# Kernel tuning notes

Hardware: AMD Instinct MI355X
Metric: run time of the kernel (lower is better)

The kernel has to match this reference:

```python
import jax, jax.numpy as jnp
import numpy as np

DIM = 1024
N_SLOTS = 64
SCALE = 1.0 / np.sqrt(DIM).astype(np.float32)


def _orthogonal(key, n, scale):
    a = jax.random.normal(key, (n, n), dtype=jnp.float32)
    q, r = jnp.linalg.qr(a)
    q = q * jnp.sign(jnp.diag(r))[None, :]
    return q * scale


def setup_inputs() -> dict:
    key = jax.random.key(0)
    ks = jax.random.split(key, 8)
    B, T, D = 16, 1024, DIM
    s = 1.0 / np.sqrt(D)
    x = jax.random.normal(ks[0], (B, T, D), dtype=jnp.float32)
    in_proj_w = jax.random.uniform(ks[1], (D, D), minval=-s, maxval=s, dtype=jnp.float32)
    out_proj_w = jax.random.uniform(ks[2], (D, D), minval=-s, maxval=s, dtype=jnp.float32)
    gate_proj_w = jax.random.uniform(ks[3], (D, D), minval=-s, maxval=s, dtype=jnp.float32)
    W_x = jax.random.uniform(ks[4], (D, D), minval=-s, maxval=s, dtype=jnp.float32)
    W_h = _orthogonal(ks[5], D, 0.9)
    W_write = jax.random.uniform(ks[6], (D, D), minval=-s, maxval=s, dtype=jnp.float32)
    b_h = jnp.zeros((D,), dtype=jnp.float32)
    return {"x": x, "in_proj_w": in_proj_w, "out_proj_w": out_proj_w,
            "gate_proj_w": gate_proj_w, "W_x": W_x, "W_h": W_h,
            "W_write": W_write, "b_h": b_h}


def _cell(x_proj, W_x, W_h, W_write, b_h):
    # x_proj: [B, T, D]
    B, T, D = x_proj.shape
    wx_all = jnp.einsum('btd,ed->bte', x_proj, W_x)  # precomputed W_x @ x
    h_tape0 = jnp.zeros((B, N_SLOTS, D), dtype=x_proj.dtype)
    h_work0 = jnp.zeros((B, D), dtype=x_proj.dtype)

    def step(carry, wx_t):
        h_tape, h_work = carry
        Rh = h_work @ W_h.T
        read_attn = jax.nn.softmax(jnp.einsum('bd,bnd->bn', h_work, h_tape) * SCALE, axis=-1)
        read = jnp.einsum('bn,bnd->bd', read_attn, h_tape)
        h_work = jnp.tanh(Rh + wx_t + read + b_h)
        write_val = h_work @ W_write.T
        write_attn = jax.nn.softmax(jnp.einsum('bd,bnd->bn', h_work, h_tape) * SCALE, axis=-1)
        wa = write_attn[..., None]  # [B, N, 1]
        h_tape = (1.0 - wa) * h_tape + wa * write_val[:, None, :]
        return (h_tape, h_work), h_work

    (h_tape_f, h_work_f), h_work_all = jax.lax.scan(
        step, (h_tape0, h_work0), jnp.swapaxes(wx_all, 0, 1))
    return jnp.swapaxes(h_work_all, 0, 1), h_tape_f, h_work_f


def reference(x, in_proj_w, out_proj_w, gate_proj_w, W_x, W_h, W_write, b_h):
    x_proj = x @ in_proj_w.T  # [B, T, D]
    h_work_all, h_tape_f, h_work_f = _cell(x_proj, W_x, W_h, W_write, b_h)
    gate = jax.nn.silu(x @ gate_proj_w.T)
    output = (h_work_all * gate) @ out_proj_w.T
    return output, h_tape_f, h_work_f
```

## Files before the change

kernel.cpp:

```cpp
#include <hip/hip_runtime.h>
#include <math.h>

#define SCALE_F 0.03125f

template<bool BT, int EPI>
__global__ __launch_bounds__(256) void gemm_nt(const float* __restrict__ A,
                                               const float* __restrict__ Bm,
                                               float* __restrict__ C,
                                               int M, int N, int K) {
  __shared__ float As[32][68];
  __shared__ float Bs[32][68];
  const int tid = threadIdx.x;
  const int n0 = blockIdx.x * 64;
  const int m0 = blockIdx.y * 64;
  const int i0 = (tid >> 4) * 4;
  const int j0 = (tid & 15) * 4;
  float acc[4][4] = {};

  for (int k0 = 0; k0 < K; k0 += 32) {
#pragma unroll
    for (int s = 0; s < 2; ++s) {
      int id = tid + 256 * s;
      int r = id >> 3, c4 = id & 7;
      float4 v = *(const float4*)&A[(size_t)(m0 + r) * K + k0 + c4 * 4];
      As[c4 * 4 + 0][r] = v.x; As[c4 * 4 + 1][r] = v.y;
      As[c4 * 4 + 2][r] = v.z; As[c4 * 4 + 3][r] = v.w;
    }
    if (BT) {
#pragma unroll
      for (int s = 0; s < 2; ++s) {
        int id = tid + 256 * s;
        int r = id >> 3, c4 = id & 7;
        float4 v = *(const float4*)&Bm[(size_t)(n0 + r) * K + k0 + c4 * 4];
        Bs[c4 * 4 + 0][r] = v.x; Bs[c4 * 4 + 1][r] = v.y;
        Bs[c4 * 4 + 2][r] = v.z; Bs[c4 * 4 + 3][r] = v.w;
      }
    } else {
#pragma unroll
      for (int s = 0; s < 2; ++s) {
        int id = tid + 256 * s;
        int kk = id >> 4, c4 = id & 15;
        float4 v = *(const float4*)&Bm[(size_t)(k0 + kk) * N + n0 + c4 * 4];
        *(float4*)&Bs[kk][c4 * 4] = v;
      }
    }
    __syncthreads();
#pragma unroll
    for (int kk = 0; kk < 32; ++kk) {
      float4 a = *(const float4*)&As[kk][i0];
      float4 b = *(const float4*)&Bs[kk][j0];
      float av[4] = {a.x, a.y, a.z, a.w};
      float bv[4] = {b.x, b.y, b.z, b.w};
#pragma unroll
      for (int ii = 0; ii < 4; ++ii)
#pragma unroll
        for (int jj = 0; jj < 4; ++jj)
          acc[ii][jj] = fmaf(av[ii], bv[jj], acc[ii][jj]);
    }
    __syncthreads();
  }

#pragma unroll
  for (int ii = 0; ii < 4; ++ii) {
    float4 v;
    float* vp = (float*)&v;
#pragma unroll
    for (int jj = 0; jj < 4; ++jj) {
      float x = acc[ii][jj];
      if (EPI == 1) x = x / (1.0f + __expf(-x));
      vp[jj] = x;
    }
    *(float4*)&C[(size_t)(m0 + i0 + ii) * N + n0 + j0] = v;
  }
}

__device__ __forceinline__ float ald(const float* p) {
  return __hip_atomic_load(p, __ATOMIC_RELAXED, __HIP_MEMORY_SCOPE_AGENT);
}
__device__ __forceinline__ void ast(float* p, float v) {
  __hip_atomic_store(p, v, __ATOMIC_RELAXED, __HIP_MEMORY_SCOPE_AGENT);
}
__device__ __forceinline__ int ildi(const int* p) {
  return __hip_atomic_load(p, __ATOMIC_RELAXED, __HIP_MEMORY_SCOPE_AGENT);
}
__device__ __forceinline__ void iast(int* p, int v) {
  __hip_atomic_store(p, v, __ATOMIC_RELAXED, __HIP_MEMORY_SCOPE_AGENT);
}

#define TIDX(n, e) ((n) * 64 + (((e) + (n)) & 63))

#define REP16(M) M(0) M(1) M(2) M(3) M(4) M(5) M(6) M(7) M(8) M(9) M(10) \
  M(11) M(12) M(13) M(14) M(15)

#define WDECL(i) float4 w##i;
#define WLOAD(i) w##i = wb4[(i)];
#define MV(i) { float4 hh; \
  hh = *(const float4*)&hs0[4*(i)]; \
  a0=fmaf(w##i.x,hh.x,a0); a0=fmaf(w##i.y,hh.y,a0); a0=fmaf(w##i.z,hh.z,a0); a0=fmaf(w##i.w,hh.w,a0); \
  hh = *(const float4*)&hs1[4*(i)]; \
  a1=fmaf(w##i.x,hh.x,a1); a1=fmaf(w##i.y,hh.y,a1); a1=fmaf(w##i.z,hh.z,a1); a1=fmaf(w##i.w,hh.w,a1); \
  hh = *(const float4*)&hs2[4*(i)]; \
  a2=fmaf(w##i.x,hh.x,a2); a2=fmaf(w##i.y,hh.y,a2); a2=fmaf(w##i.z,hh.z,a2); a2=fmaf(w##i.w,hh.w,a2); \
  hh = *(const float4*)&hs3[4*(i)]; \
  a3=fmaf(w##i.x,hh.x,a3); a3=fmaf(w##i.y,hh.y,a3); a3=fmaf(w##i.z,hh.z,a3); a3=fmaf(w##i.w,hh.w,a3); }

__global__ __launch_bounds__(512) void scan_kernel(
    const float* __restrict__ W_h, const float* __restrict__ W_wr,
    const float* __restrict__ b_h, const float* __restrict__ gate,
    float* __restrict__ wx,
    float* __restrict__ ps_g,
    float* __restrict__ Rh_g,
    float* __restrict__ wv_g,
    float* __restrict__ qp_g,
    float* __restrict__ h_g,
    float* __restrict__ tape_out,
    int* __restrict__ flags) {
  const int tid  = threadIdx.x;
  const int wg   = blockIdx.x;
  const int g    = wg >> 6;
  const int idx  = wg & 63;
  const int b_loc = idx >> 4;
  const int es   = idx & 15;
  const int gb   = g * 4;
  const int bsel = gb + b_loc;
  const int E0   = es * 64;
  const int R0   = es * 64 + b_loc * 16;
  const int wave = tid >> 6;
  const int lane = tid & 63;
  const int rl   = tid >> 4;
  const int cs   = tid & 15;
  const int nwr  = tid >> 3;
  const int ksb  = tid & 7;

  __shared__ float h_sh[4 * 1088];
  __shared__ float tape_l[64 * 64];
  __shared__ float qtmp[4][16];
  __shared__ float ws_lds[64], wa_lds[64], attn_lds[64];
  __shared__ float wv_lds[64], Rh_lds[64], h_own[64], read_lds[64];
  __shared__ float q_lds;
  __shared__ volatile float lds_pad[12288];
  lds_pad[tid] = 0.0f;

  int* fA = flags;
  int* fB = flags + 256;

  const float* Wmat = (rl < 16) ? W_h : W_wr;
  const float4* wb4 =
      (const float4*)(Wmat + (size_t)(R0 + (rl & 15)) * 1024 + cs * 64);
  REP16(WDECL)
  REP16(WLOAD)

  for (int i = tid; i < 4096; i += 512) tape_l[i] = 0.0f;

  float bh_r = 0.0f;
  if (wave == 0) bh_r = b_h[E0 + lane];
  __syncthreads();

  if (wave == 0) {
    size_t xi = (size_t)bsel * 1048576 + E0 + lane;
    float hv = tanhf(wx[xi] + bh_r);
    h_own[lane] = hv;
    ast(&h_g[bsel * 1024 + E0 + lane], hv);
    wx[xi] = hv * gate[xi];
  }
  if (tid < 64) ast(&ps_g[bsel * 1024 + es * 64 + tid], 0.0f);
  __syncthreads();
  if (tid == 0) {
    asm volatile("s_waitcnt vmcnt(0) lgkmcnt(0)" ::: "memory");
    iast(&fA[wg], 1);
  }

  const float* hs0 = &h_sh[0 * 1088 + cs * 68];
  const float* hs1 = &h_sh[1 * 1088 + cs * 68];
  const float* hs2 = &h_sh[2 * 1088 + cs * 68];
  const float* hs3 = &h_sh[3 * 1088 + cs * 68];

  for (int j = 1; j <= 1024; ++j) {
    const bool last = (j == 1024);

    if (wave == 0) {
      const int* f = &fA[g * 64];
      for (;;) {
        int v = ildi(&f[lane]);
        if (__all(v >= j)) break;
        __builtin_amdgcn_s_sleep(2);
      }
    }
    __syncthreads();

#pragma unroll
    for (int r = 0; r < 8; ++r) {
      int i = tid + r * 512;
      int bl = i >> 10, d = i & 1023;
      h_sh[bl * 1088 + (d >> 6) * 68 + (d & 63)] =
          ald(&h_g[(size_t)(gb + bl) * 1024 + d]);
    }
    float p0 = ald(&ps_g[bsel * 1024 + (ksb * 2) * 64 + nwr]);
    float p1 = ald(&ps_g[bsel * 1024 + (ksb * 2 + 1) * 64 + nwr]);
    float wxv = 0.0f, gv = 0.0f;
    size_t xj = 0;
    if (wave == 0 && !last) {
      xj  = (size_t)bsel * 1048576 + (size_t)j * 1024 + E0 + lane;
      wxv = wx[xj];
      gv  = gate[xj];
    }
    __syncthreads();

    float a0 = 0.0f, a1 = 0.0f, a2 = 0.0f, a3 = 0.0f;
    REP16(MV)
#pragma unroll
    for (int m = 1; m < 16; m <<= 1) {
      a0 += __shfl_xor(a0, m); a1 += __shfl_xor(a1, m);
      a2 += __shfl_xor(a2, m); a3 += __shfl_xor(a3, m);
    }
    if (cs == 0) {
      const int grow = R0 + (rl & 15);
      if (rl < 16) {
        ast(&Rh_g[(size_t)(gb + 0) * 1024 + grow], a0);
        ast(&Rh_g[(size_t)(gb + 1) * 1024 + grow], a1);
        ast(&Rh_g[(size_t)(gb + 2) * 1024 + grow], a2);
        ast(&Rh_g[(size_t)(gb + 3) * 1024 + grow], a3);
      } else {
        ast(&wv_g[(size_t)(gb + 0) * 1024 + grow], a0);
        ast(&wv_g[(size_t)(gb + 1) * 1024 + grow], a1);
        ast(&wv_g[(size_t)(gb + 2) * 1024 + grow], a2);
        ast(&wv_g[(size_t)(gb + 3) * 1024 + grow], a3);
        const int hoff = (grow >> 6) * 68 + (grow & 63);
        qtmp[0][rl - 16] = a0 * h_sh[0 * 1088 + hoff];
        qtmp[1][rl - 16] = a1 * h_sh[1 * 1088 + hoff];
        qtmp[2][rl - 16] = a2 * h_sh[2 * 1088 + hoff];
        qtmp[3][rl - 16] = a3 * h_sh[3 * 1088 + hoff];
      }
    }
    {
      float s = p0 + p1;
      s += __shfl_xor(s, 1);
      s += __shfl_xor(s, 2);
      s += __shfl_xor(s, 4);
      if (ksb == 0) ws_lds[nwr] = s;
    }
    __syncthreads();

    if (wave == 0) {
      float s = ws_lds[lane] * SCALE_F;
      float m = s;
#pragma unroll
      for (int off = 1; off < 64; off <<= 1) m = fmaxf(m, __shfl_xor(m, off));
      float ex = __expf(s - m);
      float sum = ex;
#pragma unroll
      for (int off = 1; off < 64; off <<= 1) sum += __shfl_xor(sum, off);
      wa_lds[lane] = ex / sum;
    } else if (wave == 1) {
      int bq = lane >> 4, k = lane & 15;
      float s = qtmp[bq][k];
      s += __shfl_xor(s, 1); s += __shfl_xor(s, 2);
      s += __shfl_xor(s, 4); s += __shfl_xor(s, 8);
      if (k == 0) ast(&qp_g[(size_t)(gb + bq) * 64 + idx], s);
    }
    __syncthreads();
    if (tid == 0) {
      asm volatile("s_waitcnt vmcnt(0) lgkmcnt(0)" ::: "memory");
      iast(&fB[wg], j);
    }

    if (wave == 0) {
      const int* f = &fB[g * 64];
      for (;;) {
        int v = ildi(&f[lane]);
        if (__all(v >= j)) break;
        __builtin_amdgcn_s_sleep(2);
      }
    }
    __syncthreads();

    if (wave == 2) {
      wv_lds[lane] = ald(&wv_g[(size_t)bsel * 1024 + E0 + lane]);
    } else if (wave == 3) {
      Rh_lds[lane] = ald(&Rh_g[(size_t)bsel * 1024 + E0 + lane]);
    } else if (wave == 1) {
      float qv = ald(&qp_g[(size_t)bsel * 64 + lane]);
#pragma unroll
      for (int off = 1; off < 64; off <<= 1) qv += __shfl_xor(qv, off);
      if (lane == 0) q_lds = qv;
    }
    __syncthreads();

    if (wave == 0 && !last) {
      float wsr = ws_lds[lane];
      float rs = fmaf(wa_lds[lane], q_lds - wsr, wsr) * SCALE_F;
      float m = rs;
#pragma unroll
      for (int off = 1; off < 64; off <<= 1) m = fmaxf(m, __shfl_xor(m, off));
      float ex = __expf(rs - m);
      float sum = ex;
#pragma unroll
      for (int off = 1; off < 64; off <<= 1) sum += __shfl_xor(sum, off);
      attn_lds[lane] = ex / sum;
    }
    {
      float wa = wa_lds[nwr];
#pragma unroll
      for (int i = 0; i < 8; ++i) {
        int e = ksb * 8 + i;
        int ix = TIDX(nwr, e);
        float t = tape_l[ix];
        tape_l[ix] = fmaf(wa, wv_lds[e] - t, t);
      }
    }
    if (last) break;
    __syncthreads();

    {
      int ge = tid >> 3, gn = tid & 7;
      float gsum = 0.0f;
#pragma unroll
      for (int i = 0; i < 8; ++i) {
        int n = gn * 8 + i;
        gsum = fmaf(attn_lds[n], tape_l[TIDX(n, ge)], gsum);
      }
      gsum += __shfl_xor(gsum, 1);
      gsum += __shfl_xor(gsum, 2);
      gsum += __shfl_xor(gsum, 4);
      if (gn == 0) read_lds[ge] = gsum;
    }
    __syncthreads();

    if (wave == 0) {
      float hv = tanhf(Rh_lds[lane] + wxv + read_lds[lane] + bh_r);
      h_own[lane] = hv;
      ast(&h_g[bsel * 1024 + E0 + lane], hv);
      wx[xj] = hv * gv;
    }
    __syncthreads();

    {
      float s = 0.0f;
#pragma unroll
      for (int i = 0; i < 8; ++i) {
        int e = ksb * 8 + i;
        s = fmaf(h_own[e], tape_l[TIDX(nwr, e)], s);
      }
      s += __shfl_xor(s, 1);
      s += __shfl_xor(s, 2);
      s += __shfl_xor(s, 4);
      if (ksb == 0) ast(&ps_g[bsel * 1024 + es * 64 + nwr], s);
    }
    __syncthreads();
    if (tid == 0) {
      asm volatile("s_waitcnt vmcnt(0) lgkmcnt(0)" ::: "memory");
      iast(&fA[wg], j + 1);
    }
  }

#pragma unroll
  for (int i = 0; i < 8; ++i) {
    int e = ksb * 8 + i;
    tape_out[(size_t)(bsel * 64 + nwr) * 1024 + E0 + e] = tape_l[TIDX(nwr, e)];
  }
}

extern "C" void kernel_launch(void* const* d_in, const int* in_sizes, int n_in,
                              void* d_out, int out_size, void* d_ws, size_t ws_size,
                              hipStream_t stream) {
  (void)in_sizes; (void)n_in; (void)out_size; (void)ws_size;
  const float* x      = (const float*)d_in[0];
  const float* in_w   = (const float*)d_in[1];
  const float* out_w  = (const float*)d_in[2];
  const float* gate_w = (const float*)d_in[3];
  const float* W_x    = (const float*)d_in[4];
  const float* W_h    = (const float*)d_in[5];
  const float* W_wr   = (const float*)d_in[6];
  const float* b_h    = (const float*)d_in[7];

  float* out  = (float*)d_out;
  float* tape = out + (size_t)16 * 1024 * 1024;
  float* hfin = tape + (size_t)16 * 64 * 1024;

  float* ws = (float*)d_ws;
  float* ps_g = ws;
  float* Rh_g = ws + 16384;
  float* wv_g = ws + 32768;
  float* qp_g = ws + 49152;
  int*   flg  = (int*)(ws + 50176);
  float* M1   = ws;
  float* wx   = ws + (1 << 20);

  float* gate = out;

  dim3 blk(256);
  gemm_nt<false, 0><<<dim3(16, 16), blk, 0, stream>>>(W_x, in_w, M1, 1024, 1024, 1024);
  gemm_nt<true, 1><<<dim3(16, 256), blk, 0, stream>>>(x, gate_w, gate, 16384, 1024, 1024);
  gemm_nt<true, 0><<<dim3(16, 256), blk, 0, stream>>>(x, M1, wx, 16384, 1024, 1024);
  hipMemsetAsync(flg, 0, 2048, stream);
  scan_kernel<<<256, 512, 0, stream>>>(W_h, W_wr, b_h, gate, wx, ps_g, Rh_g,
                                       wv_g, qp_g, hfin, tape, flg);
  gemm_nt<true, 0><<<dim3(16, 256), blk, 0, stream>>>(wx, out_w, out, 16384, 1024, 1024);
}
```

Baseline: 12.99 ms.

## Double scan block to 1024 threads with transposed h layout and per-wave row matvec

The persistent scan kernel now runs 1024 threads per block instead of 512. Each wave owns two weight rows, with lane-strided weights held in registers, and reduces across the full wave. h is stored in LDS transposed and interleaved by batch, stride 6, so each lane reads all four batch values with two float2 loads. The tape update, read and score loops are re-split across the doubled thread count. The goal is to shorten per-step latency on the serial recurrence, at the cost of longer cross-lane reductions, more threads at each barrier, and register pressure under the 1024-thread launch bound.

```diff
diff --git a/kernel.cpp b/kernel.cpp
--- a/kernel.cpp
+++ b/kernel.cpp
@@ -89,22 +89,23 @@
 
 #define TIDX(n, e) ((n) * 64 + (((e) + (n)) & 63))
 
-#define REP16(M) M(0) M(1) M(2) M(3) M(4) M(5) M(6) M(7) M(8) M(9) M(10) \
-  M(11) M(12) M(13) M(14) M(15)
-
-#define WDECL(i) float4 w##i;
-#define WLOAD(i) w##i = wb4[(i)];
-#define MV(i) { float4 hh; \
-  hh = *(const float4*)&hs0[4*(i)]; \
-  a0=fmaf(w##i.x,hh.x,a0); a0=fmaf(w##i.y,hh.y,a0); a0=fmaf(w##i.z,hh.z,a0); a0=fmaf(w##i.w,hh.w,a0); \
-  hh = *(const float4*)&hs1[4*(i)]; \
-  a1=fmaf(w##i.x,hh.x,a1); a1=fmaf(w##i.y,hh.y,a1); a1=fmaf(w##i.z,hh.z,a1); a1=fmaf(w##i.w,hh.w,a1); \
-  hh = *(const float4*)&hs2[4*(i)]; \
-  a2=fmaf(w##i.x,hh.x,a2); a2=fmaf(w##i.y,hh.y,a2); a2=fmaf(w##i.z,hh.z,a2); a2=fmaf(w##i.w,hh.w,a2); \
-  hh = *(const float4*)&hs3[4*(i)]; \
-  a3=fmaf(w##i.x,hh.x,a3); a3=fmaf(w##i.y,hh.y,a3); a3=fmaf(w##i.z,hh.z,a3); a3=fmaf(w##i.w,hh.w,a3); }
-
-__global__ __launch_bounds__(512) void scan_kernel(
+#define WQL(R, Q) \
+  float4 w##R##Q = make_float4(Wp[(R) * 1024 + 64 * (4 * (Q) + 0)], \
+                               Wp[(R) * 1024 + 64 * (4 * (Q) + 1)], \
+                               Wp[(R) * 1024 + 64 * (4 * (Q) + 2)], \
+                               Wp[(R) * 1024 + 64 * (4 * (Q) + 3)]);
+
+#define MVC(Q, IDX, COMP) { \
+  const int cc = l + 64 * (4 * (Q) + (IDX)); \
+  float2 hA = *(const float2*)&h_t[6 * cc]; \
+  float2 hB = *(const float2*)&h_t[6 * cc + 2]; \
+  a00 = fmaf(w0##Q.COMP, hA.x, a00); a01 = fmaf(w0##Q.COMP, hA.y, a01); \
+  a02 = fmaf(w0##Q.COMP, hB.x, a02); a03 = fmaf(w0##Q.COMP, hB.y, a03); \
+  a10 = fmaf(w1##Q.COMP, hA.x, a10); a11 = fmaf(w1##Q.COMP, hA.y, a11); \
+  a12 = fmaf(w1##Q.COMP, hB.x, a12); a13 = fmaf(w1##Q.COMP, hB.y, a13); }
+#define MVQ(Q) MVC(Q, 0, x) MVC(Q, 1, y) MVC(Q, 2, z) MVC(Q, 3, w)
+
+__global__ __launch_bounds__(1024) void scan_kernel(
     const float* __restrict__ W_h, const float* __restrict__ W_wr,
     const float* __restrict__ b_h, const float* __restrict__ gate,
     float* __restrict__ wx,
@@ -125,16 +126,15 @@
   const int bsel = gb + b_loc;
   const int E0   = es * 64;
   const int R0   = es * 64 + b_loc * 16;
-  const int wave = tid >> 6;
+  const int w    = tid >> 6;
   const int lane = tid & 63;
-  const int rl   = tid >> 4;
-  const int cs   = tid & 15;
-  const int nwr  = tid >> 3;
-  const int ksb  = tid & 7;
-
-  __shared__ float h_sh[4 * 1088];
+  const int l    = lane;
+  const int nw2  = tid >> 4;
+  const int ks2  = tid & 15;
+
+  __shared__ float h_t[1024 * 6];
   __shared__ float tape_l[64 * 64];
-  __shared__ float qtmp[4][16];
+  __shared__ float qtmp[8][4];
   __shared__ float ws_lds[64], wa_lds[64], attn_lds[64];
   __shared__ float wv_lds[64], Rh_lds[64], h_own[64], read_lds[64];
   __shared__ float q_lds;
@@ -144,19 +144,18 @@
   int* fA = flags;
   int* fB = flags + 256;
 
-  const float* Wmat = (rl < 16) ? W_h : W_wr;
-  const float4* wb4 =
-      (const float4*)(Wmat + (size_t)(R0 + (rl & 15)) * 1024 + cs * 64);
-  REP16(WDECL)
-  REP16(WLOAD)
-
-  for (int i = tid; i < 4096; i += 512) tape_l[i] = 0.0f;
+  const float* Wp = ((w < 8) ? W_h : W_wr)
+                    + (size_t)(R0 + ((w & 7) << 1)) * 1024 + l;
+  WQL(0, 0) WQL(0, 1) WQL(0, 2) WQL(0, 3)
+  WQL(1, 0) WQL(1, 1) WQL(1, 2) WQL(1, 3)
+
+  for (int i = tid; i < 4096; i += 1024) tape_l[i] = 0.0f;
 
   float bh_r = 0.0f;
-  if (wave == 0) bh_r = b_h[E0 + lane];
+  if (w == 0) bh_r = b_h[E0 + lane];
   __syncthreads();
 
-  if (wave == 0) {
+  if (w == 0) {
     size_t xi = (size_t)bsel * 1048576 + E0 + lane;
     float hv = tanhf(wx[xi] + bh_r);
     h_own[lane] = hv;
@@ -170,15 +169,10 @@
     iast(&fA[wg], 1);
   }
 
-  const float* hs0 = &h_sh[0 * 1088 + cs * 68];
-  const float* hs1 = &h_sh[1 * 1088 + cs * 68];
-  const float* hs2 = &h_sh[2 * 1088 + cs * 68];
-  const float* hs3 = &h_sh[3 * 1088 + cs * 68];
-
   for (int j = 1; j <= 1024; ++j) {
     const bool last = (j == 1024);
 
-    if (wave == 0) {
+    if (w == 0) {
       const int* f = &fA[g * 64];
       for (;;) {
         int v = ildi(&f[lane]);
@@ -189,59 +183,65 @@
     __syncthreads();
 
 #pragma unroll
-    for (int r = 0; r < 8; ++r) {
-      int i = tid + r * 512;
+    for (int r = 0; r < 4; ++r) {
+      int i = tid + r * 1024;
       int bl = i >> 10, d = i & 1023;
-      h_sh[bl * 1088 + (d >> 6) * 68 + (d & 63)] =
-          ald(&h_g[(size_t)(gb + bl) * 1024 + d]);
-    }
-    float p0 = ald(&ps_g[bsel * 1024 + (ksb * 2) * 64 + nwr]);
-    float p1 = ald(&ps_g[bsel * 1024 + (ksb * 2 + 1) * 64 + nwr]);
+      h_t[6 * d + bl] = ald(&h_g[(size_t)(gb + bl) * 1024 + d]);
+    }
+    float p0 = 0.0f, p1 = 0.0f;
+    if (tid < 512) {
+      int nwr = tid >> 3, ksb = tid & 7;
+      p0 = ald(&ps_g[bsel * 1024 + (ksb * 2) * 64 + nwr]);
+      p1 = ald(&ps_g[bsel * 1024 + (ksb * 2 + 1) * 64 + nwr]);
+    }
     float wxv = 0.0f, gv = 0.0f;
     size_t xj = 0;
-    if (wave == 0 && !last) {
+    if (w == 0 && !last) {
       xj  = (size_t)bsel * 1048576 + (size_t)j * 1024 + E0 + lane;
       wxv = wx[xj];
       gv  = gate[xj];
     }
     __syncthreads();
 
-    float a0 = 0.0f, a1 = 0.0f, a2 = 0.0f, a3 = 0.0f;
-    REP16(MV)
-#pragma unroll
-    for (int m = 1; m < 16; m <<= 1) {
-      a0 += __shfl_xor(a0, m); a1 += __shfl_xor(a1, m);
-      a2 += __shfl_xor(a2, m); a3 += __shfl_xor(a3, m);
-    }
-    if (cs == 0) {
-      const int grow = R0 + (rl & 15);
-      if (rl < 16) {
-        ast(&Rh_g[(size_t)(gb + 0) * 1024 + grow], a0);
-        ast(&Rh_g[(size_t)(gb + 1) * 1024 + grow], a1);
-        ast(&Rh_g[(size_t)(gb + 2) * 1024 + grow], a2);
-        ast(&Rh_g[(size_t)(gb + 3) * 1024 + grow], a3);
-      } else {
-        ast(&wv_g[(size_t)(gb + 0) * 1024 + grow], a0);
-        ast(&wv_g[(size_t)(gb + 1) * 1024 + grow], a1);
-        ast(&wv_g[(size_t)(gb + 2) * 1024 + grow], a2);
-        ast(&wv_g[(size_t)(gb + 3) * 1024 + grow], a3);
-        const int hoff = (grow >> 6) * 68 + (grow & 63);
-        qtmp[0][rl - 16] = a0 * h_sh[0 * 1088 + hoff];
-        qtmp[1][rl - 16] = a1 * h_sh[1 * 1088 + hoff];
-        qtmp[2][rl - 16] = a2 * h_sh[2 * 1088 + hoff];
-        qtmp[3][rl - 16] = a3 * h_sh[3 * 1088 + hoff];
-      }
-    }
-    {
+    float a00 = 0.0f, a01 = 0.0f, a02 = 0.0f, a03 = 0.0f;
+    float a10 = 0.0f, a11 = 0.0f, a12 = 0.0f, a13 = 0.0f;
+    MVQ(0) MVQ(1) MVQ(2) MVQ(3)
+    if (tid < 512) {
+      int nwr = tid >> 3, ksb = tid & 7;
       float s = p0 + p1;
       s += __shfl_xor(s, 1);
       s += __shfl_xor(s, 2);
       s += __shfl_xor(s, 4);
       if (ksb == 0) ws_lds[nwr] = s;
     }
-    __syncthreads();
-
-    if (wave == 0) {
+#pragma unroll
+    for (int m = 1; m < 64; m <<= 1) {
+      a00 += __shfl_xor(a00, m); a01 += __shfl_xor(a01, m);
+      a02 += __shfl_xor(a02, m); a03 += __shfl_xor(a03, m);
+      a10 += __shfl_xor(a10, m); a11 += __shfl_xor(a11, m);
+      a12 += __shfl_xor(a12, m); a13 += __shfl_xor(a13, m);
+    }
+    if (l == 0) {
+      const int gr0 = R0 + ((w & 7) << 1);
+      float* dst = (w < 8) ? Rh_g : wv_g;
+      ast(&dst[(size_t)(gb + 0) * 1024 + gr0], a00);
+      ast(&dst[(size_t)(gb + 1) * 1024 + gr0], a01);
+      ast(&dst[(size_t)(gb + 2) * 1024 + gr0], a02);
+      ast(&dst[(size_t)(gb + 3) * 1024 + gr0], a03);
+      ast(&dst[(size_t)(gb + 0) * 1024 + gr0 + 1], a10);
+      ast(&dst[(size_t)(gb + 1) * 1024 + gr0 + 1], a11);
+      ast(&dst[(size_t)(gb + 2) * 1024 + gr0 + 1], a12);
+      ast(&dst[(size_t)(gb + 3) * 1024 + gr0 + 1], a13);
+      if (w >= 8) {
+        qtmp[w - 8][0] = a00 * h_t[6 * gr0 + 0] + a10 * h_t[6 * (gr0 + 1) + 0];
+        qtmp[w - 8][1] = a01 * h_t[6 * gr0 + 1] + a11 * h_t[6 * (gr0 + 1) + 1];
+        qtmp[w - 8][2] = a02 * h_t[6 * gr0 + 2] + a12 * h_t[6 * (gr0 + 1) + 2];
+        qtmp[w - 8][3] = a03 * h_t[6 * gr0 + 3] + a13 * h_t[6 * (gr0 + 1) + 3];
+      }
+    }
+    __syncthreads();
+
+    if (w == 0) {
       float s = ws_lds[lane] * SCALE_F;
       float m = s;
 #pragma unroll
@@ -251,12 +251,15 @@
 #pragma unroll
       for (int off = 1; off < 64; off <<= 1) sum += __shfl_xor(sum, off);
       wa_lds[lane] = ex / sum;
-    } else if (wave == 1) {
-      int bq = lane >> 4, k = lane & 15;
-      float s = qtmp[bq][k];
-      s += __shfl_xor(s, 1); s += __shfl_xor(s, 2);
-      s += __shfl_xor(s, 4); s += __shfl_xor(s, 8);
-      if (k == 0) ast(&qp_g[(size_t)(gb + bq) * 64 + idx], s);
+    } else if (w == 1) {
+      if (lane < 32) {
+        int bq = lane >> 3, ww = lane & 7;
+        float s = qtmp[ww][bq];
+        s += __shfl_xor(s, 1);
+        s += __shfl_xor(s, 2);
+        s += __shfl_xor(s, 4);
+        if (ww == 0) ast(&qp_g[(size_t)(gb + bq) * 64 + idx], s);
+      }
     }
     __syncthreads();
     if (tid == 0) {
@@ -264,7 +267,7 @@
       iast(&fB[wg], j);
     }
 
-    if (wave == 0) {
+    if (w == 0) {
       const int* f = &fB[g * 64];
       for (;;) {
         int v = ildi(&f[lane]);
@@ -274,11 +277,11 @@
     }
     __syncthreads();
 
-    if (wave == 2) {
+    if (w == 2) {
       wv_lds[lane] = ald(&wv_g[(size_t)bsel * 1024 + E0 + lane]);
-    } else if (wave == 3) {
+    } else if (w == 3) {
       Rh_lds[lane] = ald(&Rh_g[(size_t)bsel * 1024 + E0 + lane]);
-    } else if (wave == 1) {
+    } else if (w == 1) {
       float qv = ald(&qp_g[(size_t)bsel * 64 + lane]);
 #pragma unroll
       for (int off = 1; off < 64; off <<= 1) qv += __shfl_xor(qv, off);
@@ -286,7 +289,7 @@
     }
     __syncthreads();
 
-    if (wave == 0 && !last) {
+    if (w == 0 && !last) {
       float wsr = ws_lds[lane];
       float rs = fmaf(wa_lds[lane], q_lds - wsr, wsr) * SCALE_F;
       float m = rs;
@@ -299,11 +302,11 @@
       attn_lds[lane] = ex / sum;
     }
     {
-      float wa = wa_lds[nwr];
-#pragma unroll
-      for (int i = 0; i < 8; ++i) {
-        int e = ksb * 8 + i;
-        int ix = TIDX(nwr, e);
+      float wa = wa_lds[nw2];
+#pragma unroll
+      for (int i = 0; i < 4; ++i) {
+        int e = ks2 * 4 + i;
+        int ix = TIDX(nw2, e);
         float t = tape_l[ix];
         tape_l[ix] = fmaf(wa, wv_lds[e] - t, t);
       }
@@ -312,21 +315,22 @@
     __syncthreads();
 
     {
-      int ge = tid >> 3, gn = tid & 7;
+      int ge = tid >> 4, gn = tid & 15;
       float gsum = 0.0f;
 #pragma unroll
-      for (int i = 0; i < 8; ++i) {
-        int n = gn * 8 + i;
+      for (int i = 0; i < 4; ++i) {
+        int n = gn * 4 + i;
         gsum = fmaf(attn_lds[n], tape_l[TIDX(n, ge)], gsum);
       }
       gsum += __shfl_xor(gsum, 1);
       gsum += __shfl_xor(gsum, 2);
       gsum += __shfl_xor(gsum, 4);
+      gsum += __shfl_xor(gsum, 8);
       if (gn == 0) read_lds[ge] = gsum;
     }
     __syncthreads();
 
-    if (wave == 0) {
+    if (w == 0) {
       float hv = tanhf(Rh_lds[lane] + wxv + read_lds[lane] + bh_r);
       h_own[lane] = hv;
       ast(&h_g[bsel * 1024 + E0 + lane], hv);
@@ -337,14 +341,15 @@
     {
       float s = 0.0f;
 #pragma unroll
-      for (int i = 0; i < 8; ++i) {
-        int e = ksb * 8 + i;
-        s = fmaf(h_own[e], tape_l[TIDX(nwr, e)], s);
+      for (int i = 0; i < 4; ++i) {
+        int e = ks2 * 4 + i;
+        s = fmaf(h_own[e], tape_l[TIDX(nw2, e)], s);
       }
       s += __shfl_xor(s, 1);
       s += __shfl_xor(s, 2);
       s += __shfl_xor(s, 4);
-      if (ksb == 0) ast(&ps_g[bsel * 1024 + es * 64 + nwr], s);
+      s += __shfl_xor(s, 8);
+      if (ks2 == 0) ast(&ps_g[bsel * 1024 + es * 64 + nw2], s);
     }
     __syncthreads();
     if (tid == 0) {
@@ -354,9 +359,9 @@
   }
 
 #pragma unroll
-  for (int i = 0; i < 8; ++i) {
-    int e = ksb * 8 + i;
-    tape_out[(size_t)(bsel * 64 + nwr) * 1024 + E0 + e] = tape_l[TIDX(nwr, e)];
+  for (int i = 0; i < 4; ++i) {
+    int e = ks2 * 4 + i;
+    tape_out[(size_t)(bsel * 64 + nw2) * 1024 + E0 + e] = tape_l[TIDX(nw2, e)];
   }
 }
 
@@ -393,7 +398,7 @@
   gemm_nt<true, 1><<<dim3(16, 256), blk, 0, stream>>>(x, gate_w, gate, 16384, 1024, 1024);
   gemm_nt<true, 0><<<dim3(16, 256), blk, 0, stream>>>(x, M1, wx, 16384, 1024, 1024);
   hipMemsetAsync(flg, 0, 2048, stream);
-  scan_kernel<<<256, 512, 0, stream>>>(W_h, W_wr, b_h, gate, wx, ps_g, Rh_g,
-                                       wv_g, qp_g, hfin, tape, flg);
+  scan_kernel<<<256, 1024, 0, stream>>>(W_h, W_wr, b_h, gate, wx, ps_g, Rh_g,
+                                        wv_g, qp_g, hfin, tape, flg);
   gemm_nt<true, 0><<<dim3(16, 256), blk, 0, stream>>>(wx, out_w, out, 16384, 1024, 1024);
 }
```

Measured after the change: 28.33 ms. 118% more time.

## Replace flag barriers with step-tagged 64-bit values in persistent scan kernel

Applied to the files above, without the earlier changes.

Replaces the per-step global flag barriers (two spin-waits plus flag stores per timestep) with 64-bit payloads that pack each float together with its step index, so consumers poll the data words directly. This removes a barrier round trip and several __syncthreads per step. The matvec is also rearranged so each thread computes both the W_h and W_write rows against a transposed h layout, and the two softmaxes are merged into one wave. The cost is twice the global traffic per value and many more polling loads, since every element is spun on individually.

```diff
diff --git a/kernel.cpp b/kernel.cpp
--- a/kernel.cpp
+++ b/kernel.cpp
@@ -74,47 +74,51 @@
   }
 }
 
-__device__ __forceinline__ float ald(const float* p) {
+typedef unsigned long long u64;
+__device__ __forceinline__ u64 ald64(const u64* p) {
   return __hip_atomic_load(p, __ATOMIC_RELAXED, __HIP_MEMORY_SCOPE_AGENT);
 }
-__device__ __forceinline__ void ast(float* p, float v) {
+__device__ __forceinline__ void ast64(u64* p, u64 v) {
   __hip_atomic_store(p, v, __ATOMIC_RELAXED, __HIP_MEMORY_SCOPE_AGENT);
 }
-__device__ __forceinline__ int ildi(const int* p) {
-  return __hip_atomic_load(p, __ATOMIC_RELAXED, __HIP_MEMORY_SCOPE_AGENT);
-}
-__device__ __forceinline__ void iast(int* p, int v) {
-  __hip_atomic_store(p, v, __ATOMIC_RELAXED, __HIP_MEMORY_SCOPE_AGENT);
+__device__ __forceinline__ u64 pk(float v, int j) {
+  return ((u64)(unsigned)j << 32) | (u64)__float_as_uint(v);
+}
+__device__ __forceinline__ float pollv(const u64* p, int j) {
+  u64 u = ald64(p);
+  while ((unsigned)(u >> 32) != (unsigned)j) {
+    __builtin_amdgcn_s_sleep(1);
+    u = ald64(p);
+  }
+  return __uint_as_float((unsigned)u);
 }
 
 #define TIDX(n, e) ((n) * 64 + (((e) + (n)) & 63))
 
-#define REP16(M) M(0) M(1) M(2) M(3) M(4) M(5) M(6) M(7) M(8) M(9) M(10) \
-  M(11) M(12) M(13) M(14) M(15)
-
-#define WDECL(i) float4 w##i;
-#define WLOAD(i) w##i = wb4[(i)];
-#define MV(i) { float4 hh; \
-  hh = *(const float4*)&hs0[4*(i)]; \
-  a0=fmaf(w##i.x,hh.x,a0); a0=fmaf(w##i.y,hh.y,a0); a0=fmaf(w##i.z,hh.z,a0); a0=fmaf(w##i.w,hh.w,a0); \
-  hh = *(const float4*)&hs1[4*(i)]; \
-  a1=fmaf(w##i.x,hh.x,a1); a1=fmaf(w##i.y,hh.y,a1); a1=fmaf(w##i.z,hh.z,a1); a1=fmaf(w##i.w,hh.w,a1); \
-  hh = *(const float4*)&hs2[4*(i)]; \
-  a2=fmaf(w##i.x,hh.x,a2); a2=fmaf(w##i.y,hh.y,a2); a2=fmaf(w##i.z,hh.z,a2); a2=fmaf(w##i.w,hh.w,a2); \
-  hh = *(const float4*)&hs3[4*(i)]; \
-  a3=fmaf(w##i.x,hh.x,a3); a3=fmaf(w##i.y,hh.y,a3); a3=fmaf(w##i.z,hh.z,a3); a3=fmaf(w##i.w,hh.w,a3); }
+#define REP32(M) M(0) M(1) M(2) M(3) M(4) M(5) M(6) M(7) M(8) M(9) M(10) \
+  M(11) M(12) M(13) M(14) M(15) M(16) M(17) M(18) M(19) M(20) M(21) M(22) \
+  M(23) M(24) M(25) M(26) M(27) M(28) M(29) M(30) M(31)
+
+#define RW(i) const float wh##i = Whp[32 * (i)]; \
+              const float ww##i = Wwp[32 * (i)];
+#define MVI(i) { float4 hh = ht4[cseg + 32 * (i)]; \
+  ah0 = fmaf(wh##i, hh.x, ah0); ah1 = fmaf(wh##i, hh.y, ah1); \
+  ah2 = fmaf(wh##i, hh.z, ah2); ah3 = fmaf(wh##i, hh.w, ah3); \
+  aw0 = fmaf(ww##i, hh.x, aw0); aw1 = fmaf(ww##i, hh.y, aw1); \
+  aw2 = fmaf(ww##i, hh.z, aw2); aw3 = fmaf(ww##i, hh.w, aw3); }
 
 __global__ __launch_bounds__(512) void scan_kernel(
     const float* __restrict__ W_h, const float* __restrict__ W_wr,
     const float* __restrict__ b_h, const float* __restrict__ gate,
     float* __restrict__ wx,
-    float* __restrict__ ps_g,
-    float* __restrict__ Rh_g,
-    float* __restrict__ wv_g,
-    float* __restrict__ qp_g,
-    float* __restrict__ h_g,
-    float* __restrict__ tape_out,
-    int* __restrict__ flags) {
+    u64* __restrict__ h2,
+    u64* __restrict__ ps2,
+    u64* __restrict__ Rh2,
+    u64* __restrict__ wv2,
+    u64* __restrict__ qp2,
+    float* __restrict__ hfin,
+    float* __restrict__ tape_out)
+{
   const int tid  = threadIdx.x;
   const int wg   = blockIdx.x;
   const int g    = wg >> 6;
@@ -125,113 +129,64 @@
   const int bsel = gb + b_loc;
   const int E0   = es * 64;
   const int R0   = es * 64 + b_loc * 16;
-  const int wave = tid >> 6;
+  const int w    = tid >> 6;
   const int lane = tid & 63;
-  const int rl   = tid >> 4;
-  const int cs   = tid & 15;
+  const int row  = tid >> 5;
+  const int cseg = tid & 31;
+  const int gr   = R0 + row;
   const int nwr  = tid >> 3;
   const int ksb  = tid & 7;
 
-  __shared__ float h_sh[4 * 1088];
-  __shared__ float tape_l[64 * 64];
-  __shared__ float qtmp[4][16];
+  __shared__ float h_t[4096];
+  __shared__ float tape_l[4096];
+  __shared__ float qtmp[16][4];
   __shared__ float ws_lds[64], wa_lds[64], attn_lds[64];
   __shared__ float wv_lds[64], Rh_lds[64], h_own[64], read_lds[64];
-  __shared__ float q_lds;
   __shared__ volatile float lds_pad[12288];
-  lds_pad[tid] = 0.0f;
-
-  int* fA = flags;
-  int* fB = flags + 256;
-
-  const float* Wmat = (rl < 16) ? W_h : W_wr;
-  const float4* wb4 =
-      (const float4*)(Wmat + (size_t)(R0 + (rl & 15)) * 1024 + cs * 64);
-  REP16(WDECL)
-  REP16(WLOAD)
+  lds_pad[tid] = 0.0f; lds_pad[tid + 512] = 0.0f;
+
+  const float* Whp = W_h + (size_t)gr * 1024 + cseg;
+  const float* Wwp = W_wr + (size_t)gr * 1024 + cseg;
+  REP32(RW)
+
+  const float4* ht4 = (const float4*)h_t;
 
   for (int i = tid; i < 4096; i += 512) tape_l[i] = 0.0f;
 
   float bh_r = 0.0f;
-  if (wave == 0) bh_r = b_h[E0 + lane];
+  if (w == 0) bh_r = b_h[E0 + lane];
   __syncthreads();
 
-  if (wave == 0) {
+  if (w == 0) {
     size_t xi = (size_t)bsel * 1048576 + E0 + lane;
     float hv = tanhf(wx[xi] + bh_r);
     h_own[lane] = hv;
-    ast(&h_g[bsel * 1024 + E0 + lane], hv);
+    ast64(&h2[(size_t)bsel * 1024 + E0 + lane], pk(hv, 1));
     wx[xi] = hv * gate[xi];
   }
-  if (tid < 64) ast(&ps_g[bsel * 1024 + es * 64 + tid], 0.0f);
+  if (tid < 64) ast64(&ps2[(size_t)bsel * 1024 + es * 64 + tid], pk(0.0f, 1));
   __syncthreads();
-  if (tid == 0) {
-    asm volatile("s_waitcnt vmcnt(0) lgkmcnt(0)" ::: "memory");
-    iast(&fA[wg], 1);
-  }
-
-  const float* hs0 = &h_sh[0 * 1088 + cs * 68];
-  const float* hs1 = &h_sh[1 * 1088 + cs * 68];
-  const float* hs2 = &h_sh[2 * 1088 + cs * 68];
-  const float* hs3 = &h_sh[3 * 1088 + cs * 68];
 
   for (int j = 1; j <= 1024; ++j) {
     const bool last = (j == 1024);
-
-    if (wave == 0) {
-      const int* f = &fA[g * 64];
-      for (;;) {
-        int v = ildi(&f[lane]);
-        if (__all(v >= j)) break;
-        __builtin_amdgcn_s_sleep(2);
-      }
-    }
-    __syncthreads();
 
 #pragma unroll
     for (int r = 0; r < 8; ++r) {
       int i = tid + r * 512;
       int bl = i >> 10, d = i & 1023;
-      h_sh[bl * 1088 + (d >> 6) * 68 + (d & 63)] =
-          ald(&h_g[(size_t)(gb + bl) * 1024 + d]);
-    }
-    float p0 = ald(&ps_g[bsel * 1024 + (ksb * 2) * 64 + nwr]);
-    float p1 = ald(&ps_g[bsel * 1024 + (ksb * 2 + 1) * 64 + nwr]);
+      h_t[4 * d + bl] = pollv(&h2[(size_t)(gb + bl) * 1024 + d], j);
+    }
+    float p0 = pollv(&ps2[(size_t)bsel * 1024 + (ksb * 2) * 64 + nwr], j);
+    float p1 = pollv(&ps2[(size_t)bsel * 1024 + (ksb * 2 + 1) * 64 + nwr], j);
     float wxv = 0.0f, gv = 0.0f;
     size_t xj = 0;
-    if (wave == 0 && !last) {
+    if (w == 0 && !last) {
       xj  = (size_t)bsel * 1048576 + (size_t)j * 1024 + E0 + lane;
       wxv = wx[xj];
       gv  = gate[xj];
     }
     __syncthreads();
 
-    float a0 = 0.0f, a1 = 0.0f, a2 = 0.0f, a3 = 0.0f;
-    REP16(MV)
-#pragma unroll
-    for (int m = 1; m < 16; m <<= 1) {
-      a0 += __shfl_xor(a0, m); a1 += __shfl_xor(a1, m);
-      a2 += __shfl_xor(a2, m); a3 += __shfl_xor(a3, m);
-    }
-    if (cs == 0) {
-      const int grow = R0 + (rl & 15);
-      if (rl < 16) {
-        ast(&Rh_g[(size_t)(gb + 0) * 1024 + grow], a0);
-        ast(&Rh_g[(size_t)(gb + 1) * 1024 + grow], a1);
-        ast(&Rh_g[(size_t)(gb + 2) * 1024 + grow], a2);
-        ast(&Rh_g[(size_t)(gb + 3) * 1024 + grow], a3);
-      } else {
-        ast(&wv_g[(size_t)(gb + 0) * 1024 + grow], a0);
-        ast(&wv_g[(size_t)(gb + 1) * 1024 + grow], a1);
-        ast(&wv_g[(size_t)(gb + 2) * 1024 + grow], a2);
-        ast(&wv_g[(size_t)(gb + 3) * 1024 + grow], a3);
-        const int hoff = (grow >> 6) * 68 + (grow & 63);
-        qtmp[0][rl - 16] = a0 * h_sh[0 * 1088 + hoff];
-        qtmp[1][rl - 16] = a1 * h_sh[1 * 1088 + hoff];
-        qtmp[2][rl - 16] = a2 * h_sh[2 * 1088 + hoff];
-        qtmp[3][rl - 16] = a3 * h_sh[3 * 1088 + hoff];
-      }
-    }
     {
       float s = p0 + p1;
       s += __shfl_xor(s, 1);
@@ -239,9 +194,33 @@
       s += __shfl_xor(s, 4);
       if (ksb == 0) ws_lds[nwr] = s;
     }
-    __syncthreads();
-
-    if (wave == 0) {
+    float ah0 = 0.0f, ah1 = 0.0f, ah2 = 0.0f, ah3 = 0.0f;
+    float aw0 = 0.0f, aw1 = 0.0f, aw2 = 0.0f, aw3 = 0.0f;
+    REP32(MVI)
+#pragma unroll
+    for (int m = 1; m < 32; m <<= 1) {
+      ah0 += __shfl_xor(ah0, m); ah1 += __shfl_xor(ah1, m);
+      ah2 += __shfl_xor(ah2, m); ah3 += __shfl_xor(ah3, m);
+      aw0 += __shfl_xor(aw0, m); aw1 += __shfl_xor(aw1, m);
+      aw2 += __shfl_xor(aw2, m); aw3 += __shfl_xor(aw3, m);
+    }
+    if (cseg == 0) {
+      ast64(&Rh2[(size_t)(gb + 0) * 1024 + gr], pk(ah0, j));
+      ast64(&Rh2[(size_t)(gb + 1) * 1024 + gr], pk(ah1, j));
+      ast64(&Rh2[(size_t)(gb + 2) * 1024 + gr], pk(ah2, j));
+      ast64(&Rh2[(size_t)(gb + 3) * 1024 + gr], pk(ah3, j));
+      ast64(&wv2[(size_t)(gb + 0) * 1024 + gr], pk(aw0, j));
+      ast64(&wv2[(size_t)(gb + 1) * 1024 + gr], pk(aw1, j));
+      ast64(&wv2[(size_t)(gb + 2) * 1024 + gr], pk(aw2, j));
+      ast64(&wv2[(size_t)(gb + 3) * 1024 + gr], pk(aw3, j));
+      qtmp[row][0] = aw0 * h_t[4 * gr + 0];
+      qtmp[row][1] = aw1 * h_t[4 * gr + 1];
+      qtmp[row][2] = aw2 * h_t[4 * gr + 2];
+      qtmp[row][3] = aw3 * h_t[4 * gr + 3];
+    }
+    __syncthreads();
+
+    if (w == 0) {
       float s = ws_lds[lane] * SCALE_F;
       float m = s;
 #pragma unroll
@@ -251,53 +230,43 @@
 #pragma unroll
       for (int off = 1; off < 64; off <<= 1) sum += __shfl_xor(sum, off);
       wa_lds[lane] = ex / sum;
-    } else if (wave == 1) {
-      int bq = lane >> 4, k = lane & 15;
-      float s = qtmp[bq][k];
+    } else if (w == 1) {
+      int bq = lane >> 4, r = lane & 15;
+      float s = qtmp[r][bq];
       s += __shfl_xor(s, 1); s += __shfl_xor(s, 2);
       s += __shfl_xor(s, 4); s += __shfl_xor(s, 8);
-      if (k == 0) ast(&qp_g[(size_t)(gb + bq) * 64 + idx], s);
-    }
-    __syncthreads();
-    if (tid == 0) {
-      asm volatile("s_waitcnt vmcnt(0) lgkmcnt(0)" ::: "memory");
-      iast(&fB[wg], j);
-    }
-
-    if (wave == 0) {
-      const int* f = &fB[g * 64];
-      for (;;) {
-        int v = ildi(&f[lane]);
-        if (__all(v >= j)) break;
-        __builtin_amdgcn_s_sleep(2);
-      }
-    }
-    __syncthreads();
-
-    if (wave == 2) {
-      wv_lds[lane] = ald(&wv_g[(size_t)bsel * 1024 + E0 + lane]);
-    } else if (wave == 3) {
-      Rh_lds[lane] = ald(&Rh_g[(size_t)bsel * 1024 + E0 + lane]);
-    } else if (wave == 1) {
-      float qv = ald(&qp_g[(size_t)bsel * 64 + lane]);
+      if (r == 0) ast64(&qp2[(size_t)(gb + bq) * 64 + idx], pk(s, j));
+      float qv = pollv(&qp2[(size_t)bsel * 64 + lane], j);
 #pragma unroll
       for (int off = 1; off < 64; off <<= 1) qv += __shfl_xor(qv, off);
-      if (lane == 0) q_lds = qv;
-    }
-    __syncthreads();
-
-    if (wave == 0 && !last) {
-      float wsr = ws_lds[lane];
-      float rs = fmaf(wa_lds[lane], q_lds - wsr, wsr) * SCALE_F;
-      float m = rs;
-#pragma unroll
-      for (int off = 1; off < 64; off <<= 1) m = fmaxf(m, __shfl_xor(m, off));
-      float ex = __expf(rs - m);
-      float sum = ex;
-#pragma unroll
-      for (int off = 1; off < 64; off <<= 1) sum += __shfl_xor(sum, off);
-      attn_lds[lane] = ex / sum;
-    }
+      if (!last) {
+        float wsr = ws_lds[lane];
+        float sm = wsr * SCALE_F;
+        float m = sm;
+#pragma unroll
+        for (int off = 1; off < 64; off <<= 1) m = fmaxf(m, __shfl_xor(m, off));
+        float ex = __expf(sm - m);
+        float sum = ex;
+#pragma unroll
+        for (int off = 1; off < 64; off <<= 1) sum += __shfl_xor(sum, off);
+        float wa_l = ex / sum;
+        float rs = fmaf(wa_l, qv - wsr, wsr) * SCALE_F;
+        float m2 = rs;
+#pragma unroll
+        for (int off = 1; off < 64; off <<= 1) m2 = fmaxf(m2, __shfl_xor(m2, off));
+        float ex2 = __expf(rs - m2);
+        float sum2 = ex2;
+#pragma unroll
+        for (int off = 1; off < 64; off <<= 1) sum2 += __shfl_xor(sum2, off);
+        attn_lds[lane] = ex2 / sum2;
+      }
+    } else if (w == 2) {
+      wv_lds[lane] = pollv(&wv2[(size_t)bsel * 1024 + E0 + lane], j);
+    } else if (w == 3) {
+      Rh_lds[lane] = pollv(&Rh2[(size_t)bsel * 1024 + E0 + lane], j);
+    }
+    __syncthreads();
+
     {
       float wa = wa_lds[nwr];
 #pragma unroll
@@ -326,10 +295,10 @@
     }
     __syncthreads();
 
-    if (wave == 0) {
+    if (w == 0) {
       float hv = tanhf(Rh_lds[lane] + wxv + read_lds[lane] + bh_r);
       h_own[lane] = hv;
-      ast(&h_g[bsel * 1024 + E0 + lane], hv);
+      ast64(&h2[(size_t)bsel * 1024 + E0 + lane], pk(hv, j + 1));
       wx[xj] = hv * gv;
     }
     __syncthreads();
@@ -344,12 +313,7 @@
       s += __shfl_xor(s, 1);
       s += __shfl_xor(s, 2);
       s += __shfl_xor(s, 4);
-      if (ksb == 0) ast(&ps_g[bsel * 1024 + es * 64 + nwr], s);
-    }
-    __syncthreads();
-    if (tid == 0) {
-      asm volatile("s_waitcnt vmcnt(0) lgkmcnt(0)" ::: "memory");
-      iast(&fA[wg], j + 1);
+      if (ksb == 0) ast64(&ps2[(size_t)bsel * 1024 + es * 64 + nwr], pk(s, j + 1));
     }
   }
 
@@ -358,6 +322,7 @@
     int e = ksb * 8 + i;
     tape_out[(size_t)(bsel * 64 + nwr) * 1024 + E0 + e] = tape_l[TIDX(nwr, e)];
   }
+  if (w == 0) hfin[(size_t)bsel * 1024 + E0 + lane] = h_own[lane];
 }
 
 extern "C" void kernel_launch(void* const* d_in, const int* in_sizes, int n_in,
@@ -378,13 +343,13 @@
   float* hfin = tape + (size_t)16 * 64 * 1024;
 
   float* ws = (float*)d_ws;
-  float* ps_g = ws;
-  float* Rh_g = ws + 16384;
-  float* wv_g = ws + 32768;
-  float* qp_g = ws + 49152;
-  int*   flg  = (int*)(ws + 50176);
-  float* M1   = ws;
-  float* wx   = ws + (1 << 20);
+  u64* h2  = (u64*)ws;
+  u64* ps2 = (u64*)(ws + 32768);
+  u64* Rh2 = (u64*)(ws + 65536);
+  u64* wv2 = (u64*)(ws + 98304);
+  u64* qp2 = (u64*)(ws + 131072);
+  float* M1 = ws;
+  float* wx = ws + (1 << 20);
 
   float* gate = out;
 
@@ -392,8 +357,8 @@
   gemm_nt<false, 0><<<dim3(16, 16), blk, 0, stream>>>(W_x, in_w, M1, 1024, 1024, 1024);
   gemm_nt<true, 1><<<dim3(16, 256), blk, 0, stream>>>(x, gate_w, gate, 16384, 1024, 1024);
   gemm_nt<true, 0><<<dim3(16, 256), blk, 0, stream>>>(x, M1, wx, 16384, 1024, 1024);
-  hipMemsetAsync(flg, 0, 2048, stream);
-  scan_kernel<<<256, 512, 0, stream>>>(W_h, W_wr, b_h, gate, wx, ps_g, Rh_g,
-                                       wv_g, qp_g, hfin, tape, flg);
+  hipMemsetAsync(ws, 0, 133120 * sizeof(float), stream);
+  scan_kernel<<<256, 512, 0, stream>>>(W_h, W_wr, b_h, gate, wx, h2, ps2,
+                                       Rh2, wv2, qp2, hfin, tape);
   gemm_nt<true, 0><<<dim3(16, 256), blk, 0, stream>>>(wx, out_w, out, 16384, 1024, 1024);
 }
```

Measured after the change: 10.94 ms. 15.8% less time.
